# Kernel optimization log

Measured on AMD Instinct MI355X. Metric: run time of the kernel, lower is better.

## Reference

```python
import jax, jax.numpy as jnp
import numpy as np

R = 32  # voxel grid resolution
EPS = 0.0


def setup_inputs() -> dict:
    key = jax.random.key(0)
    k1, k2 = jax.random.split(key)
    B, C, N = 8, 64, 65536
    features = jax.random.normal(k1, (B, C, N), dtype=jnp.float32)
    coords = jax.random.normal(k2, (B, 3, N), dtype=jnp.float32)
    return {"features": features, "coords": coords}


def _voxelize_coords(coords):
    # coords: [B, 3, N] -> normalized coords [B,3,N] and voxel indices [B,3,N]
    coords = jax.lax.stop_gradient(coords)  # torch: coords.detach()
    nc = coords - coords.mean(axis=2, keepdims=True)
    # normalize=True branch
    norms = jnp.linalg.norm(nc, axis=1, keepdims=True)        # [B,1,N]
    max_norm = norms.max(axis=2, keepdims=True)               # [B,1,1]
    nc = nc / (max_norm * 2.0 + EPS) + 0.5
    nc = jnp.clip(nc * R, 0.0, R - 1)
    vox = jnp.round(nc).astype(jnp.int32)                     # [B,3,N]
    return nc, vox


def _avg_voxelize(features, vox):
    # features: [B, C, N]; vox: [B, 3, N] int -> [B, C, R, R, R]
    B, C, N = features.shape
    flat = vox[:, 0] * (R * R) + vox[:, 1] * R + vox[:, 2]    # [B, N]
    seg = (flat + jnp.arange(B, dtype=jnp.int32)[:, None] * (R ** 3)).reshape(-1)
    feats = features.transpose(0, 2, 1).reshape(B * N, C)      # [B*N, C]
    sums = jax.ops.segment_sum(feats, seg, num_segments=B * R ** 3)          # [B*R^3, C]
    counts = jax.ops.segment_sum(jnp.ones((B * N,), features.dtype), seg,
                                 num_segments=B * R ** 3)                     # [B*R^3]
    avg = sums / jnp.maximum(counts, 1.0)[:, None]
    return avg.reshape(B, R ** 3, C).transpose(0, 2, 1).reshape(B, C, R, R, R)


def reference(features, coords):
    nc, vox = _voxelize_coords(coords)
    out = _avg_voxelize(features, vox)
    return out, nc
```

## Files before the change

### kernel.cpp

```cpp
#include <hip/hip_runtime.h>
#include <hip/hip_bf16.h>
#include <cstdint>

static constexpr int B_  = 8;
static constexpr int C_  = 64;
static constexpr int N_  = 65536;
static constexpr int Rr  = 32;
static constexpr int R3  = Rr * Rr * Rr;
static constexpr int PBLK = 16;
static constexpr int PTS_PER_BLK = N_ / PBLK;

__device__ __forceinline__ float bf2f(unsigned short u) {
    union { unsigned int i; float f; } x;
    x.i = ((unsigned int)u) << 16;
    return x.f;
}

__global__ void zero_counts_kernel(int4* __restrict__ counts) {
    counts[blockIdx.x * 256 + threadIdx.x] = make_int4(0, 0, 0, 0);
}

__global__ void partial_mean_kernel(const float* __restrict__ coords,
                                    float* __restrict__ pmean) {
    const int blk = blockIdx.x & (PBLK - 1);
    const int ba  = blockIdx.x / PBLK;
    const float4* p = (const float4*)(coords + (size_t)ba * N_ + (size_t)blk * PTS_PER_BLK);
    float s = 0.f;
    #pragma unroll
    for (int k = 0; k < PTS_PER_BLK / 4 / 256; ++k) {
        float4 v = p[k * 256 + threadIdx.x];
        s += (v.x + v.y) + (v.z + v.w);
    }
    #pragma unroll
    for (int off = 32; off >= 1; off >>= 1) s += __shfl_down(s, off, 64);
    __shared__ float sm[4];
    if ((threadIdx.x & 63) == 0) sm[threadIdx.x >> 6] = s;
    __syncthreads();
    if (threadIdx.x == 0) pmean[blockIdx.x] = sm[0] + sm[1] + sm[2] + sm[3];
}

__global__ void partial_max_kernel(const float* __restrict__ coords,
                                   const float* __restrict__ pmean,
                                   float* __restrict__ pmax) {
    const int blk = blockIdx.x & (PBLK - 1);
    const int b   = blockIdx.x / PBLK;
    __shared__ float msh[3];
    if (threadIdx.x == 0) {
        #pragma unroll
        for (int a = 0; a < 3; ++a) {
            float t = 0.f;
            #pragma unroll
            for (int k = 0; k < PBLK; ++k) t += pmean[(b * 3 + a) * PBLK + k];
            msh[a] = t / (float)N_;
        }
    }
    __syncthreads();
    const float mx = msh[0], my = msh[1], mz = msh[2];
    const float4* px = (const float4*)(coords + (size_t)b * 3 * N_ + (size_t)blk * PTS_PER_BLK);
    const float4* py = px + N_ / 4;
    const float4* pz = px + 2 * (N_ / 4);
    float m = 0.f;
    #pragma unroll
    for (int k = 0; k < PTS_PER_BLK / 4 / 256; ++k) {
        const int i = k * 256 + threadIdx.x;
        float4 x = px[i], y = py[i], z = pz[i];
        float x0 = x.x - mx, y0 = y.x - my, z0 = z.x - mz;
        float x1 = x.y - mx, y1 = y.y - my, z1 = z.y - mz;
        float x2 = x.z - mx, y2 = y.z - my, z2 = z.z - mz;
        float x3 = x.w - mx, y3 = y.w - my, z3 = z.w - mz;
        m = fmaxf(m, x0 * x0 + y0 * y0 + z0 * z0);
        m = fmaxf(m, x1 * x1 + y1 * y1 + z1 * z1);
        m = fmaxf(m, x2 * x2 + y2 * y2 + z2 * z2);
        m = fmaxf(m, x3 * x3 + y3 * y3 + z3 * z3);
    }
    #pragma unroll
    for (int off = 32; off >= 1; off >>= 1) m = fmaxf(m, __shfl_down(m, off, 64));
    __shared__ float sm[4];
    if ((threadIdx.x & 63) == 0) sm[threadIdx.x >> 6] = m;
    __syncthreads();
    if (threadIdx.x == 0)
        pmax[blockIdx.x] = fmaxf(fmaxf(sm[0], sm[1]), fmaxf(sm[2], sm[3]));
}

__global__ void voxelize_kernel(const float* __restrict__ coords,
                                const float* __restrict__ pmean,
                                const float* __restrict__ pmax,
                                float* __restrict__ nc_out,
                                int* __restrict__ flat_out,
                                int* __restrict__ counts) {
    const int idx = blockIdx.x * blockDim.x + threadIdx.x;
    const int b = idx >> 16;
    const int n = idx & (N_ - 1);
    __shared__ float par[4];
    if (threadIdx.x == 0) {
        #pragma unroll
        for (int a = 0; a < 3; ++a) {
            float t = 0.f;
            #pragma unroll
            for (int k = 0; k < PBLK; ++k) t += pmean[(b * 3 + a) * PBLK + k];
            par[a] = t / (float)N_;
        }
        float mm = 0.f;
        #pragma unroll
        for (int k = 0; k < PBLK; ++k) mm = fmaxf(mm, pmax[b * PBLK + k]);
        par[3] = 2.0f * sqrtf(mm);
    }
    __syncthreads();
    const float* pc = coords + (size_t)b * 3 * N_;
    const float denom = par[3];
    int flat = 0;
    #pragma unroll
    for (int a = 0; a < 3; ++a) {
        float v = (pc[(size_t)a * N_ + n] - par[a]) / denom + 0.5f;
        v = v * (float)Rr;
        v = fminf(fmaxf(v, 0.0f), (float)(Rr - 1));
        nc_out[(size_t)b * 3 * N_ + (size_t)a * N_ + n] = v;
        flat = flat * Rr + (int)rintf(v);
    }
    flat_out[idx] = flat;
    atomicAdd(&counts[b * R3 + flat], 1);
}

__global__ void scan_kernel(const int* __restrict__ counts,
                            int* __restrict__ cursor) {
    const int b = blockIdx.x;
    const int t = threadIdx.x;
    constexpr int PER = R3 / 1024;
    int local[PER];
    int s = 0;
    #pragma unroll
    for (int k = 0; k < PER; ++k) { local[k] = counts[b * R3 + t * PER + k]; s += local[k]; }
    __shared__ int sm[1024];
    sm[t] = s;
    __syncthreads();
    for (int off = 1; off < 1024; off <<= 1) {
        int v = (t >= off) ? sm[t - off] : 0;
        __syncthreads();
        sm[t] += v;
        __syncthreads();
    }
    int run = sm[t] - s;
    #pragma unroll
    for (int k = 0; k < PER; ++k) { cursor[b * R3 + t * PER + k] = run; run += local[k]; }
}

__global__ void scatter_ids_kernel(const int* __restrict__ flat,
                                   int* __restrict__ cursor,
                                   int* __restrict__ pos) {
    const int idx = blockIdx.x * blockDim.x + threadIdx.x;
    if (idx >= B_ * N_) return;
    const int b = idx >> 16;
    const int f = flat[idx];
    pos[idx] = atomicAdd(&cursor[b * R3 + f], 1);
}

template<typename T>
__global__ void sorted_transpose_kernel(const float* __restrict__ features,
                                        const int* __restrict__ pos,
                                        T* __restrict__ ftS) {
    const int tile = blockIdx.x & 1023;
    const int b    = blockIdx.x >> 10;
    const int n0   = tile * 64;
    __shared__ float tileS[64][65];
    __shared__ int pos_s[64];
    const int lane = threadIdx.x & 63, row0 = threadIdx.x >> 6;
    if (threadIdx.x < 64) pos_s[threadIdx.x] = pos[(size_t)b * N_ + n0 + threadIdx.x];
    #pragma unroll
    for (int it = 0; it < 16; ++it) {
        const int c = row0 + it * 4;
        tileS[c][lane] = features[((size_t)b * C_ + c) * N_ + n0 + lane];
    }
    __syncthreads();
    #pragma unroll
    for (int it = 0; it < 16; ++it) {
        const int j = row0 + it * 4;
        ftS[((size_t)b * N_ + pos_s[j]) * C_ + lane] = (T)tileS[lane][j];
    }
}

__global__ void voxel_sum_kernel(const __hip_bfloat16* __restrict__ ftS,
                                 const int* __restrict__ counts,
                                 const int* __restrict__ cursor,
                                 float* __restrict__ acc) {
    const int wid  = (blockIdx.x * blockDim.x + threadIdx.x) >> 6;
    const int lane = threadIdx.x & 63;
    if (wid >= B_ * R3) return;
    const int b = wid >> 15;
    const int cnt = counts[wid];
    if (cnt == 0) return;
    const int start = cursor[wid] - cnt;
    const int sub = lane >> 4;
    const int g   = lane & 15;
    const unsigned short* base =
        (const unsigned short*)ftS + ((size_t)b * N_ + start) * C_ + g * 4;
    float a0 = 0.f, a1 = 0.f, a2 = 0.f, a3 = 0.f;
    for (int t = sub; t < cnt; t += 4) {
        const ushort4 u = *(const ushort4*)(base + (size_t)t * C_);
        a0 += bf2f(u.x); a1 += bf2f(u.y); a2 += bf2f(u.z); a3 += bf2f(u.w);
    }
    #pragma unroll
    for (int off = 16; off <= 32; off <<= 1) {
        a0 += __shfl_xor(a0, off, 64);
        a1 += __shfl_xor(a1, off, 64);
        a2 += __shfl_xor(a2, off, 64);
        a3 += __shfl_xor(a3, off, 64);
    }
    if (sub == 0) {
        float4 r = make_float4(a0, a1, a2, a3);
        *(float4*)(acc + ((size_t)wid) * C_ + g * 4) = r;
    }
}

__global__ void transpose_finalize_kernel(const float* __restrict__ acc,
                                          const int* __restrict__ counts,
                                          float* __restrict__ out) {
    const int chunk = blockIdx.x;
    const int b  = chunk >> 9;
    const int v0 = (chunk & 511) * 64;
    __shared__ float tile[64][65];
    __shared__ float cnt_s[64];
    __shared__ int   occ[64];
    const int lane = threadIdx.x & 63, row0 = threadIdx.x >> 6;
    if (threadIdx.x < 64) {
        const int c = counts[b * R3 + v0 + threadIdx.x];
        occ[threadIdx.x]   = c;
        cnt_s[threadIdx.x] = fmaxf((float)c, 1.0f);
    }
    __syncthreads();
    #pragma unroll
    for (int it = 0; it < 16; ++it) {
        const int vi = row0 + it * 4;
        tile[vi][lane] = occ[vi] ? acc[((size_t)(b * R3 + v0 + vi)) * C_ + lane] : 0.f;
    }
    __syncthreads();
    #pragma unroll
    for (int it = 0; it < 16; ++it) {
        const int c = row0 + it * 4;
        out[((size_t)b * C_ + c) * R3 + v0 + lane] = tile[lane][c] / cnt_s[lane];
    }
}

__global__ void mean_kernel(const float* __restrict__ coords,
                            float* __restrict__ mean_out) {
    const int ba = blockIdx.x;
    const float* p = coords + (size_t)ba * N_;
    float s = 0.f;
    for (int i = threadIdx.x; i < N_; i += blockDim.x) s += p[i];
    #pragma unroll
    for (int off = 32; off >= 1; off >>= 1) s += __shfl_down(s, off, 64);
    __shared__ float sm[4];
    if ((threadIdx.x & 63) == 0) sm[threadIdx.x >> 6] = s;
    __syncthreads();
    if (threadIdx.x == 0) mean_out[ba] = (sm[0] + sm[1] + sm[2] + sm[3]) / (float)N_;
}

__global__ void maxnorm_kernel(const float* __restrict__ coords,
                               const float* __restrict__ mean,
                               float* __restrict__ maxn) {
    const int b = blockIdx.x;
    const float* p = coords + (size_t)b * 3 * N_;
    const float mx = mean[b * 3 + 0], my = mean[b * 3 + 1], mz = mean[b * 3 + 2];
    float m = 0.f;
    for (int i = threadIdx.x; i < N_; i += blockDim.x) {
        const float x = p[i] - mx, y = p[N_ + i] - my, z = p[2 * N_ + i] - mz;
        m = fmaxf(m, x * x + y * y + z * z);
    }
    #pragma unroll
    for (int off = 32; off >= 1; off >>= 1) m = fmaxf(m, __shfl_down(m, off, 64));
    __shared__ float sm[16];
    if ((threadIdx.x & 63) == 0) sm[threadIdx.x >> 6] = m;
    __syncthreads();
    if (threadIdx.x == 0) {
        float t = sm[0];
        const int nw = blockDim.x >> 6;
        for (int w = 1; w < nw; ++w) t = fmaxf(t, sm[w]);
        maxn[b] = sqrtf(t);
    }
}

__global__ void scatter_kernel(const float* __restrict__ coords,
                               const float* __restrict__ features,
                               const float* __restrict__ mean,
                               const float* __restrict__ maxn,
                               float* __restrict__ out,
                               float* __restrict__ nc_out,
                               float* __restrict__ counts) {
    const int idx = blockIdx.x * blockDim.x + threadIdx.x;
    if (idx >= B_ * N_) return;
    const int b = idx >> 16;
    const int n = idx & (N_ - 1);
    const float* pc = coords + (size_t)b * 3 * N_;
    const float denom = 2.0f * maxn[b];
    int flat = 0;
    #pragma unroll
    for (int a = 0; a < 3; ++a) {
        float v = (pc[(size_t)a * N_ + n] - mean[b * 3 + a]) / denom + 0.5f;
        v = v * (float)Rr;
        v = fminf(fmaxf(v, 0.0f), (float)(Rr - 1));
        nc_out[(size_t)b * 3 * N_ + (size_t)a * N_ + n] = v;
        flat = flat * Rr + (int)rintf(v);
    }
    atomicAdd(&counts[b * R3 + flat], 1.0f);
    const float* pf = features + (size_t)b * C_ * N_ + n;
    float* po = out + (size_t)b * C_ * R3 + flat;
    #pragma unroll 4
    for (int c = 0; c < C_; ++c) atomicAdd(po + (size_t)c * R3, pf[(size_t)c * N_]);
}

__global__ void finalize_kernel(float* __restrict__ out,
                                const float* __restrict__ counts) {
    const int idx = blockIdx.x * blockDim.x + threadIdx.x;
    if (idx >= B_ * C_ * R3) return;
    const int b = idx / (C_ * R3);
    const int v = idx & (R3 - 1);
    out[idx] = out[idx] / fmaxf(counts[b * R3 + v], 1.0f);
}

extern "C" void kernel_launch(void* const* d_in, const int* in_sizes, int n_in,
                              void* d_out, int out_size, void* d_ws, size_t ws_size,
                              hipStream_t stream) {
    const float* features = (const float*)d_in[0];
    const float* coords   = (const float*)d_in[1];

    float* out    = (float*)d_out;
    float* nc_out = out + (size_t)B_ * C_ * R3;

    const size_t accB  = (size_t)B_ * R3 * C_ * sizeof(float);
    const size_t cntB  = (size_t)B_ * R3 * sizeof(int);
    const size_t curB  = cntB;
    const size_t flatB = (size_t)B_ * N_ * sizeof(int);
    const size_t posB  = flatB;
    const size_t smallB = 4096;
    const size_t ftsBf16B = (size_t)B_ * N_ * C_ * sizeof(__hip_bfloat16);

    const size_t need = accB + cntB + curB + flatB + posB + smallB + ftsBf16B;
    const int pts = B_ * N_;

    if (ws_size >= need) {
        char* w = (char*)d_ws;
        float* acc        = (float*)w;                 w += accB;
        int*   counts     = (int*)w;                   w += cntB;
        int*   cursor     = (int*)w;                   w += curB;
        int*   flat       = (int*)w;                   w += flatB;
        int*   pos        = (int*)w;                   w += posB;
        float* pmean      = (float*)w;
        float* pmax       = pmean + B_ * 3 * PBLK;
        w += smallB;
        __hip_bfloat16* ftS = (__hip_bfloat16*)w;

        zero_counts_kernel<<<cntB / (256 * 16), 256, 0, stream>>>((int4*)counts);

        partial_mean_kernel<<<B_ * 3 * PBLK, 256, 0, stream>>>(coords, pmean);
        partial_max_kernel<<<B_ * PBLK, 256, 0, stream>>>(coords, pmean, pmax);
        voxelize_kernel<<<pts / 256, 256, 0, stream>>>(
            coords, pmean, pmax, nc_out, flat, counts);
        scan_kernel<<<B_, 1024, 0, stream>>>(counts, cursor);
        scatter_ids_kernel<<<(pts + 255) / 256, 256, 0, stream>>>(flat, cursor, pos);
        sorted_transpose_kernel<__hip_bfloat16><<<B_ * (N_ / 64), 256, 0, stream>>>(
            features, pos, ftS);
        voxel_sum_kernel<<<(B_ * R3) / 4, 256, 0, stream>>>(ftS, counts, cursor, acc);
        transpose_finalize_kernel<<<B_ * (R3 / 64), 256, 0, stream>>>(acc, counts, out);
    } else {
        float* counts = (float*)d_ws;
        float* mean   = counts + (size_t)B_ * R3;
        float* maxn   = mean + B_ * 3;

        hipMemsetAsync(d_out, 0, (size_t)B_ * C_ * R3 * sizeof(float), stream);
        hipMemsetAsync(d_ws, 0, ((size_t)B_ * R3 + B_ * 3 + B_) * sizeof(float), stream);

        mean_kernel<<<B_ * 3, 256, 0, stream>>>(coords, mean);
        maxnorm_kernel<<<B_, 1024, 0, stream>>>(coords, mean, maxn);
        scatter_kernel<<<(pts + 255) / 256, 256, 0, stream>>>(
            coords, features, mean, maxn, out, nc_out, counts);
        finalize_kernel<<<(B_ * C_ * R3 + 255) / 256, 256, 0, stream>>>(out, counts);
    }
}
```

Before: 196.5 us.

## Fuse zeroing/id scatter, compact occupied voxels, vectorize bf16 transpose

Folds count zeroing into the partial-mean launch. Merges the position-assigning atomic pass into the sorted transpose kernel, which now converts to bf16 in shared memory and writes 16-byte packed rows. The scan also builds a compacted list of occupied voxels, so the summation kernel grid-strides only over non-empty voxels instead of launching a wave per voxel. The aim is fewer launches, no pos buffer round-trip, wider stores and no idle empty-voxel waves. The cost is a second scan pass, a global atomic, and list entries whose order depends on block timing.

```diff
diff --git a/kernel.cpp b/kernel.cpp
--- a/kernel.cpp
+++ b/kernel.cpp
@@ -15,13 +15,21 @@
     x.i = ((unsigned int)u) << 16;
     return x.f;
 }
-
-__global__ void zero_counts_kernel(int4* __restrict__ counts) {
-    counts[blockIdx.x * 256 + threadIdx.x] = make_int4(0, 0, 0, 0);
-}
-
-__global__ void partial_mean_kernel(const float* __restrict__ coords,
-                                    float* __restrict__ pmean) {
+__device__ __forceinline__ unsigned short f2bf(float f) {
+    __hip_bfloat16 h = (__hip_bfloat16)f;
+    return *reinterpret_cast<unsigned short*>(&h);
+}
+
+__global__ void pmean_zero_kernel(const float* __restrict__ coords,
+                                  float* __restrict__ pmean,
+                                  int4* __restrict__ counts4,
+                                  int* __restrict__ n_occ) {
+    if (blockIdx.x >= B_ * 3 * PBLK) {
+        const int zb = blockIdx.x - B_ * 3 * PBLK;
+        counts4[zb * 256 + threadIdx.x] = make_int4(0, 0, 0, 0);
+        if (zb == 0 && threadIdx.x == 0) *n_occ = 0;
+        return;
+    }
     const int blk = blockIdx.x & (PBLK - 1);
     const int ba  = blockIdx.x / PBLK;
     const float4* p = (const float4*)(coords + (size_t)ba * N_ + (size_t)blk * PTS_PER_BLK);
@@ -121,16 +129,23 @@
     atomicAdd(&counts[b * R3 + flat], 1);
 }
 
-__global__ void scan_kernel(const int* __restrict__ counts,
-                            int* __restrict__ cursor) {
+__global__ void scan_compact_kernel(const int* __restrict__ counts,
+                                    int* __restrict__ cursor,
+                                    int4* __restrict__ clist,
+                                    int* __restrict__ n_occ) {
     const int b = blockIdx.x;
     const int t = threadIdx.x;
     constexpr int PER = R3 / 1024;
     int local[PER];
-    int s = 0;
-    #pragma unroll
-    for (int k = 0; k < PER; ++k) { local[k] = counts[b * R3 + t * PER + k]; s += local[k]; }
+    int s = 0, nz = 0;
+    #pragma unroll
+    for (int k = 0; k < PER; ++k) {
+        local[k] = counts[b * R3 + t * PER + k];
+        s += local[k];
+        if (local[k] > 0) nz++;
+    }
     __shared__ int sm[1024];
+    __shared__ int basesh;
     sm[t] = s;
     __syncthreads();
     for (int off = 1; off < 1024; off <<= 1) {
@@ -139,75 +154,101 @@
         sm[t] += v;
         __syncthreads();
     }
-    int run = sm[t] - s;
-    #pragma unroll
-    for (int k = 0; k < PER; ++k) { cursor[b * R3 + t * PER + k] = run; run += local[k]; }
-}
-
-__global__ void scatter_ids_kernel(const int* __restrict__ flat,
-                                   int* __restrict__ cursor,
-                                   int* __restrict__ pos) {
-    const int idx = blockIdx.x * blockDim.x + threadIdx.x;
-    if (idx >= B_ * N_) return;
-    const int b = idx >> 16;
-    const int f = flat[idx];
-    pos[idx] = atomicAdd(&cursor[b * R3 + f], 1);
-}
-
-template<typename T>
-__global__ void sorted_transpose_kernel(const float* __restrict__ features,
-                                        const int* __restrict__ pos,
-                                        T* __restrict__ ftS) {
+    const int run0 = sm[t] - s;
+    __syncthreads();
+    sm[t] = nz;
+    __syncthreads();
+    for (int off = 1; off < 1024; off <<= 1) {
+        int v = (t >= off) ? sm[t - off] : 0;
+        __syncthreads();
+        sm[t] += v;
+        __syncthreads();
+    }
+    if (t == 0) basesh = atomicAdd(n_occ, sm[1023]);
+    __syncthreads();
+    int slot = basesh + sm[t] - nz;
+    int run = run0;
+    #pragma unroll
+    for (int k = 0; k < PER; ++k) {
+        const int v = t * PER + k;
+        cursor[b * R3 + v] = run;
+        if (local[k] > 0) clist[slot++] = make_int4(b * R3 + v, run, local[k], 0);
+        run += local[k];
+    }
+}
+
+__global__ void sorted_transpose_ids_kernel(const float* __restrict__ features,
+                                            const int* __restrict__ flat,
+                                            int* __restrict__ cursor,
+                                            __hip_bfloat16* __restrict__ ftS) {
     const int tile = blockIdx.x & 1023;
     const int b    = blockIdx.x >> 10;
     const int n0   = tile * 64;
-    __shared__ float tileS[64][65];
+    __shared__ unsigned short tileS[64][66];
     __shared__ int pos_s[64];
-    const int lane = threadIdx.x & 63, row0 = threadIdx.x >> 6;
-    if (threadIdx.x < 64) pos_s[threadIdx.x] = pos[(size_t)b * N_ + n0 + threadIdx.x];
-    #pragma unroll
-    for (int it = 0; it < 16; ++it) {
-        const int c = row0 + it * 4;
-        tileS[c][lane] = features[((size_t)b * C_ + c) * N_ + n0 + lane];
-    }
-    __syncthreads();
-    #pragma unroll
-    for (int it = 0; it < 16; ++it) {
-        const int j = row0 + it * 4;
-        ftS[((size_t)b * N_ + pos_s[j]) * C_ + lane] = (T)tileS[lane][j];
-    }
-}
-
-__global__ void voxel_sum_kernel(const __hip_bfloat16* __restrict__ ftS,
-                                 const int* __restrict__ counts,
-                                 const int* __restrict__ cursor,
-                                 float* __restrict__ acc) {
-    const int wid  = (blockIdx.x * blockDim.x + threadIdx.x) >> 6;
+    const int t = threadIdx.x;
+    if (t < 64) {
+        const int f = flat[b * N_ + n0 + t];
+        pos_s[t] = atomicAdd(&cursor[b * R3 + f], 1);
+    }
+    const int g  = t & 15;
+    const int c0 = t >> 4;
+    #pragma unroll
+    for (int it = 0; it < 4; ++it) {
+        const int c = it * 16 + c0;
+        const float4 v = *(const float4*)(features + ((size_t)b * C_ + c) * N_ + n0 + g * 4);
+        ushort4 u;
+        u.x = f2bf(v.x); u.y = f2bf(v.y); u.z = f2bf(v.z); u.w = f2bf(v.w);
+        *(ushort4*)&tileS[c][g * 4] = u;
+    }
+    __syncthreads();
+    #pragma unroll
+    for (int p = 0; p < 2; ++p) {
+        const int oi = p * 256 + t;
+        const int j  = oi >> 3;
+        const int o  = oi & 7;
+        unsigned int w0, w1, w2, w3;
+        const int cb = o * 8;
+        w0 = (unsigned int)tileS[cb + 0][j] | ((unsigned int)tileS[cb + 1][j] << 16);
+        w1 = (unsigned int)tileS[cb + 2][j] | ((unsigned int)tileS[cb + 3][j] << 16);
+        w2 = (unsigned int)tileS[cb + 4][j] | ((unsigned int)tileS[cb + 5][j] << 16);
+        w3 = (unsigned int)tileS[cb + 6][j] | ((unsigned int)tileS[cb + 7][j] << 16);
+        uint4 w = make_uint4(w0, w1, w2, w3);
+        *(uint4*)((unsigned short*)ftS + ((size_t)b * N_ + pos_s[j]) * C_ + cb) = w;
+    }
+}
+
+__global__ void voxel_sum_compact_kernel(const __hip_bfloat16* __restrict__ ftS,
+                                         const int4* __restrict__ clist,
+                                         const int* __restrict__ n_occ,
+                                         float* __restrict__ acc) {
     const int lane = threadIdx.x & 63;
-    if (wid >= B_ * R3) return;
-    const int b = wid >> 15;
-    const int cnt = counts[wid];
-    if (cnt == 0) return;
-    const int start = cursor[wid] - cnt;
+    const int gw = blockIdx.x * (blockDim.x >> 6) + (threadIdx.x >> 6);
+    const int nw = gridDim.x * (blockDim.x >> 6);
+    const int tot = *n_occ;
     const int sub = lane >> 4;
     const int g   = lane & 15;
-    const unsigned short* base =
-        (const unsigned short*)ftS + ((size_t)b * N_ + start) * C_ + g * 4;
-    float a0 = 0.f, a1 = 0.f, a2 = 0.f, a3 = 0.f;
-    for (int t = sub; t < cnt; t += 4) {
-        const ushort4 u = *(const ushort4*)(base + (size_t)t * C_);
-        a0 += bf2f(u.x); a1 += bf2f(u.y); a2 += bf2f(u.z); a3 += bf2f(u.w);
-    }
-    #pragma unroll
-    for (int off = 16; off <= 32; off <<= 1) {
-        a0 += __shfl_xor(a0, off, 64);
-        a1 += __shfl_xor(a1, off, 64);
-        a2 += __shfl_xor(a2, off, 64);
-        a3 += __shfl_xor(a3, off, 64);
-    }
-    if (sub == 0) {
-        float4 r = make_float4(a0, a1, a2, a3);
-        *(float4*)(acc + ((size_t)wid) * C_ + g * 4) = r;
+    for (int e = gw; e < tot; e += nw) {
+        const int4 ent = clist[e];
+        const int wid = ent.x, start = ent.y, cnt = ent.z;
+        const int b = wid >> 15;
+        const unsigned short* base =
+            (const unsigned short*)ftS + ((size_t)b * N_ + start) * C_ + g * 4;
+        float a0 = 0.f, a1 = 0.f, a2 = 0.f, a3 = 0.f;
+        for (int t = sub; t < cnt; t += 4) {
+            const ushort4 u = *(const ushort4*)(base + (size_t)t * C_);
+            a0 += bf2f(u.x); a1 += bf2f(u.y); a2 += bf2f(u.z); a3 += bf2f(u.w);
+        }
+        #pragma unroll
+        for (int off = 16; off <= 32; off <<= 1) {
+            a0 += __shfl_xor(a0, off, 64);
+            a1 += __shfl_xor(a1, off, 64);
+            a2 += __shfl_xor(a2, off, 64);
+            a3 += __shfl_xor(a3, off, 64);
+        }
+        if (sub == 0) {
+            *(float4*)(acc + (size_t)wid * C_ + g * 4) = make_float4(a0, a1, a2, a3);
+        }
     }
 }
 
@@ -325,40 +366,39 @@
     float* out    = (float*)d_out;
     float* nc_out = out + (size_t)B_ * C_ * R3;
 
-    const size_t accB  = (size_t)B_ * R3 * C_ * sizeof(float);
-    const size_t cntB  = (size_t)B_ * R3 * sizeof(int);
-    const size_t curB  = cntB;
-    const size_t flatB = (size_t)B_ * N_ * sizeof(int);
-    const size_t posB  = flatB;
+    const size_t accB   = (size_t)B_ * R3 * C_ * sizeof(float);
+    const size_t cntB   = (size_t)B_ * R3 * sizeof(int);
+    const size_t curB   = cntB;
+    const size_t flatB  = (size_t)B_ * N_ * sizeof(int);
+    const size_t clistB = (size_t)B_ * R3 * sizeof(int4);
     const size_t smallB = 4096;
-    const size_t ftsBf16B = (size_t)B_ * N_ * C_ * sizeof(__hip_bfloat16);
-
-    const size_t need = accB + cntB + curB + flatB + posB + smallB + ftsBf16B;
+    const size_t ftsB   = (size_t)B_ * N_ * C_ * sizeof(__hip_bfloat16);
+
+    const size_t need = accB + cntB + curB + flatB + clistB + smallB + ftsB;
     const int pts = B_ * N_;
 
     if (ws_size >= need) {
         char* w = (char*)d_ws;
-        float* acc        = (float*)w;                 w += accB;
-        int*   counts     = (int*)w;                   w += cntB;
-        int*   cursor     = (int*)w;                   w += curB;
-        int*   flat       = (int*)w;                   w += flatB;
-        int*   pos        = (int*)w;                   w += posB;
-        float* pmean      = (float*)w;
-        float* pmax       = pmean + B_ * 3 * PBLK;
+        float* acc    = (float*)w;                 w += accB;
+        int*   counts = (int*)w;                   w += cntB;
+        int*   cursor = (int*)w;                   w += curB;
+        int*   flat   = (int*)w;                   w += flatB;
+        int4*  clist  = (int4*)w;                  w += clistB;
+        int*   n_occ  = (int*)w;
+        float* pmean  = (float*)(w + 16);
+        float* pmax   = pmean + B_ * 3 * PBLK;
         w += smallB;
         __hip_bfloat16* ftS = (__hip_bfloat16*)w;
 
-        zero_counts_kernel<<<cntB / (256 * 16), 256, 0, stream>>>((int4*)counts);
-
-        partial_mean_kernel<<<B_ * 3 * PBLK, 256, 0, stream>>>(coords, pmean);
+        pmean_zero_kernel<<<B_ * 3 * PBLK + 256, 256, 0, stream>>>(
+            coords, pmean, (int4*)counts, n_occ);
         partial_max_kernel<<<B_ * PBLK, 256, 0, stream>>>(coords, pmean, pmax);
         voxelize_kernel<<<pts / 256, 256, 0, stream>>>(
             coords, pmean, pmax, nc_out, flat, counts);
-        scan_kernel<<<B_, 1024, 0, stream>>>(counts, cursor);
-        scatter_ids_kernel<<<(pts + 255) / 256, 256, 0, stream>>>(flat, cursor, pos);
-        sorted_transpose_kernel<__hip_bfloat16><<<B_ * (N_ / 64), 256, 0, stream>>>(
-            features, pos, ftS);
-        voxel_sum_kernel<<<(B_ * R3) / 4, 256, 0, stream>>>(ftS, counts, cursor, acc);
+        scan_compact_kernel<<<B_, 1024, 0, stream>>>(counts, cursor, clist, n_occ);
+        sorted_transpose_ids_kernel<<<B_ * (N_ / 64), 256, 0, stream>>>(
+            features, flat, cursor, ftS);
+        voxel_sum_compact_kernel<<<512, 256, 0, stream>>>(ftS, clist, n_occ, acc);
         transpose_finalize_kernel<<<B_ * (R3 / 64), 256, 0, stream>>>(acc, counts, out);
     } else {
         float* counts = (float*)d_ws;
```

After: 201.3 us. 2.4% more time.
